# Optimization experiments

Hardware: AMD Instinct MI355X
Metric: run time of the kernel (lower is better)

## Reference

```python
import jax, jax.numpy as jnp
import numpy as np

B, H, W, D = 16, 56, 56, 384
NH, WS, SH = 12, 7, 3
HD = D // NH
N = WS * WS
nW = (H // WS) * (W // WS)
L = H * W

def _rel_pos_index():
    c = np.stack(np.meshgrid(np.arange(WS), np.arange(WS), indexing='ij')).reshape(2, -1)
    r = (c[:, :, None] - c[:, None, :]).transpose(1, 2, 0)
    r[:, :, 0] += WS - 1
    r[:, :, 1] += WS - 1
    r[:, :, 0] *= 2 * WS - 1
    return r.sum(-1)  # (N, N) int indices into bias table

RPI = _rel_pos_index()

def _attn_mask():
    img = np.zeros((H, W))
    cnt = 0
    sl = (slice(0, H - WS), slice(H - WS, H - SH), slice(H - SH, None))
    for hs in sl:
        for ws in sl:
            img[hs, ws] = cnt
            cnt += 1
    mw = img.reshape(H // WS, WS, W // WS, WS).transpose(0, 2, 1, 3).reshape(-1, N)
    am = mw[:, None, :] - mw[:, :, None]
    return np.where(am != 0, -100.0, 0.0).astype(np.float32)  # (nW, N, N)

AM = jnp.asarray(_attn_mask())

def _ln(x, g, b):
    m = jnp.mean(x, -1, keepdims=True)
    v = jnp.mean((x - m) ** 2, -1, keepdims=True)
    return (x - m) * jax.lax.rsqrt(v + 1e-5) * g + b

def _fwd(x, norm1_g, norm1_b, qkv_w, qkv_b, rpb, proj_w, proj_b, norm2_g, norm2_b,
         fc1_w, fc1_b, fc2_w, fc2_b, expand_w, exnorm_g, exnorm_b):
    def blk(x, i, shifted):
        sc = x
        h = _ln(x, norm1_g[i], norm1_b[i]).reshape(B, H, W, D)
        if shifted:
            h = jnp.roll(h, (-SH, -SH), axis=(1, 2))
        # window partition: (B*nW, N, D)
        xw = h.reshape(B, H // WS, WS, W // WS, WS, D).transpose(0, 1, 3, 2, 4, 5).reshape(-1, N, D)
        qkv = (xw @ qkv_w[i] + qkv_b[i]).reshape(-1, N, 3, NH, HD).transpose(2, 0, 3, 1, 4)
        q, k, v = qkv[0] * HD ** -0.5, qkv[1], qkv[2]
        bias = rpb[i][RPI].transpose(2, 0, 1)  # (NH, N, N)
        attn = jnp.einsum('bhid,bhjd->bhij', q, k) + bias[None]
        if shifted:
            attn = (attn.reshape(B, nW, NH, N, N) + AM[None, :, None]).reshape(-1, NH, N, N)
        attn = jax.nn.softmax(attn, axis=-1)
        o = jnp.einsum('bhij,bhjd->bhid', attn, v).transpose(0, 2, 1, 3).reshape(-1, N, D)
        o = o @ proj_w[i] + proj_b[i]
        # window reverse: (B, H, W, D)
        o = o.reshape(B, H // WS, W // WS, WS, WS, D).transpose(0, 1, 3, 2, 4, 5).reshape(B, H, W, D)
        if shifted:
            o = jnp.roll(o, (SH, SH), axis=(1, 2))
        x = sc + o.reshape(B, L, D)
        h2 = _ln(x, norm2_g[i], norm2_b[i])
        h2 = jax.nn.gelu(h2 @ fc1_w[i] + fc1_b[i], approximate=False) @ fc2_w[i] + fc2_b[i]
        return x + h2

    x = blk(x, 0, False)  # W-MSA
    x = blk(x, 1, True)   # SW-MSA
    # PatchExpand: dim -> 2*dim, pixel-shuffle 2x2, norm(dim/2)
    xe = (x @ expand_w).reshape(B, H, W, 2, 2, D // 2)
    xe = xe.transpose(0, 1, 3, 2, 4, 5).reshape(B, 4 * L, D // 2)
    return _ln(xe, exnorm_g, exnorm_b)

def setup_inputs() -> dict:
    ks = jax.random.split(jax.random.key(0), 8)
    r = lambda k, s: jax.random.normal(k, s, jnp.float32) * 0.02
    return {
        'x': jax.random.normal(ks[0], (B, L, D), jnp.float32),
        'norm1_g': jnp.ones((2, D)), 'norm1_b': jnp.zeros((2, D)),
        'qkv_w': r(ks[1], (2, D, 3 * D)), 'qkv_b': jnp.zeros((2, 3 * D)),
        'rpb': r(ks[2], (2, (2 * WS - 1) ** 2, NH)),
        'proj_w': r(ks[3], (2, D, D)), 'proj_b': jnp.zeros((2, D)),
        'norm2_g': jnp.ones((2, D)), 'norm2_b': jnp.zeros((2, D)),
        'fc1_w': r(ks[4], (2, D, 4 * D)), 'fc1_b': jnp.zeros((2, 4 * D)),
        'fc2_w': r(ks[5], (2, 4 * D, D)), 'fc2_b': jnp.zeros((2, D)),
        'expand_w': r(ks[6], (D, 2 * D)),
        'exnorm_g': jnp.ones((D // 2,)), 'exnorm_b': jnp.zeros((D // 2,)),
    }

def reference(x, norm1_g, norm1_b, qkv_w, qkv_b, rpb, proj_w, proj_b, norm2_g, norm2_b,
              fc1_w, fc1_b, fc2_w, fc2_b, expand_w, exnorm_g, exnorm_b):
    return _fwd(x, norm1_g, norm1_b, qkv_w, qkv_b, rpb, proj_w, proj_b, norm2_g, norm2_b,
                fc1_w, fc1_b, fc2_w, fc2_b, expand_w, exnorm_g, exnorm_b)
```

## Files before the change

### kernel.cpp

```cpp
#include <hip/hip_runtime.h>
#include <cstdint>
#include <cstddef>

typedef unsigned short u16;
typedef unsigned int u32;
typedef __attribute__((ext_vector_type(8))) short bf16x8;
typedef __attribute__((ext_vector_type(4))) float f32x4;

__device__ __forceinline__ float bf2f(u32 u) {
  union { u32 i; float f; } c; c.i = u << 16; return c.f;
}
__device__ __forceinline__ u16 f2bf(float f) {
  union { float f; u32 i; } c; c.f = f;
  u32 r = c.i + 0x7fffu + ((c.i >> 16) & 1u);
  return (u16)(r >> 16);
}

__device__ __forceinline__ int srcrow_map(int m, int shifted) {
  int w = m / 49, n = m - w * 49;
  int b = w >> 6, wi = w & 63;
  int wy = wi >> 3, wx = wi & 7;
  int ty = n / 7, tx = n - ty * 7;
  int h = wy * 7 + ty, x = wx * 7 + tx;
  if (shifted) { h += 3; if (h >= 56) h -= 56; x += 3; if (x >= 56) x -= 56; }
  return b * 3136 + h * 56 + x;
}

__global__ void detect_kernel(const u32* __restrict__ x, int* __restrict__ flag) {
  int t = threadIdx.x;
  int c = 0;
  for (int i = t; i < 1024; i += 256) {
    u32 e = (x[i] >> 7) & 0xFFu;
    c += (e >= 100 && e <= 130) ? 1 : 0;
  }
#pragma unroll
  for (int m = 1; m < 64; m <<= 1) c += __shfl_xor(c, m, 64);
  __shared__ int part[4];
  if ((t & 63) == 0) part[t >> 6] = c;
  __syncthreads();
  if (t == 0) flag[0] = (part[0] + part[1] + part[2] + part[3] > 700) ? 1 : 0;
}

__global__ void convert_kernel(const void* __restrict__ in, u16* __restrict__ out,
                               int n, const int* __restrict__ flag) {
  int i = blockIdx.x * 256 + threadIdx.x;
  if (i >= n) return;
  if (flag[0]) out[i] = ((const u16*)in)[i];
  else out[i] = f2bf(((const float*)in)[i]);
}

__global__ void transpose_kernel(const void* __restrict__ in, u16* __restrict__ out,
                                 int R, int C, int total, const int* __restrict__ flag) {
  int i = blockIdx.x * 256 + threadIdx.x;
  if (i >= total) return;
  int rc = R * C;
  int bb = i / rc, rem = i - bb * rc;
  int c = rem / R, r = rem - c * R;
  size_t s = (size_t)bb * rc + (size_t)r * C + c;
  out[i] = flag[0] ? ((const u16*)in)[s] : f2bf(((const float*)in)[s]);
}

__global__ __launch_bounds__(256)
void ln384_kernel(const u16* __restrict__ in, const u16* __restrict__ g,
                  const u16* __restrict__ b, u16* __restrict__ out) {
  int row = blockIdx.x * 4 + (threadIdx.x >> 6);
  int lane = threadIdx.x & 63;
  const u32* p = (const u32*)(in + (size_t)row * 384);
  float x[6]; float sum = 0.f, sq = 0.f;
#pragma unroll
  for (int j = 0; j < 3; ++j) {
    u32 u = p[lane + 64 * j];
    float a0 = bf2f(u & 0xffff), a1 = bf2f(u >> 16);
    x[2 * j] = a0; x[2 * j + 1] = a1;
    sum += a0 + a1; sq += a0 * a0 + a1 * a1;
  }
#pragma unroll
  for (int m = 1; m < 64; m <<= 1) { sum += __shfl_xor(sum, m, 64); sq += __shfl_xor(sq, m, 64); }
  float mean = sum * (1.f / 384.f);
  float var = sq * (1.f / 384.f) - mean * mean;
  float rstd = rsqrtf(var + 1e-5f);
  u32* op = (u32*)(out + (size_t)row * 384);
  const u32* g32 = (const u32*)g; const u32* b32 = (const u32*)b;
#pragma unroll
  for (int j = 0; j < 3; ++j) {
    int c = lane + 64 * j;
    u32 gg = g32[c], bb = b32[c];
    float y0 = (x[2 * j] - mean) * rstd * bf2f(gg & 0xffff) + bf2f(bb & 0xffff);
    float y1 = (x[2 * j + 1] - mean) * rstd * bf2f(gg >> 16) + bf2f(bb >> 16);
    op[c] = (u32)f2bf(y0) | ((u32)f2bf(y1) << 16);
  }
}

__global__ __launch_bounds__(256)
void lnfinal_kernel(const u16* __restrict__ in, const u16* __restrict__ g,
                    const u16* __restrict__ b, void* __restrict__ outv,
                    const int* __restrict__ flag) {
  int row = blockIdx.x * 8 + (threadIdx.x >> 5);
  int s = threadIdx.x & 31;
  int fl = flag[0];
  int bb = row / 12544, rem = row - bb * 12544;
  int hh = rem / 112, wp = rem - hh * 112;
  int h = hh >> 1, a = hh & 1, w = wp >> 1, c2 = wp & 1;
  const u32* p = (const u32*)(in + ((size_t)(bb * 3136 + h * 56 + w)) * 768 + (a * 2 + c2) * 192);
  float x[6]; float sum = 0.f, sq = 0.f;
#pragma unroll
  for (int j = 0; j < 3; ++j) {
    u32 u = p[s + 32 * j];
    float a0 = bf2f(u & 0xffff), a1 = bf2f(u >> 16);
    x[2 * j] = a0; x[2 * j + 1] = a1;
    sum += a0 + a1; sq += a0 * a0 + a1 * a1;
  }
#pragma unroll
  for (int m = 1; m < 32; m <<= 1) { sum += __shfl_xor(sum, m, 32); sq += __shfl_xor(sq, m, 32); }
  float mean = sum * (1.f / 192.f);
  float var = sq * (1.f / 192.f) - mean * mean;
  float rstd = rsqrtf(var + 1e-5f);
  const u32* g32 = (const u32*)g; const u32* b32 = (const u32*)b;
#pragma unroll
  for (int j = 0; j < 3; ++j) {
    int c = s + 32 * j;
    u32 gg = g32[c], bv = b32[c];
    float y0 = (x[2 * j] - mean) * rstd * bf2f(gg & 0xffff) + bf2f(bv & 0xffff);
    float y1 = (x[2 * j + 1] - mean) * rstd * bf2f(gg >> 16) + bf2f(bv >> 16);
    if (fl) {
      u32* op = (u32*)((u16*)outv + (size_t)row * 192);
      op[c] = (u32)f2bf(y0) | ((u32)f2bf(y1) << 16);
    } else {
      float2* op = (float2*)((float*)outv + (size_t)row * 192);
      float2 v; v.x = y0; v.y = y1;
      op[c] = v;
    }
  }
}

template <int MODE>
__global__ __launch_bounds__(256, 2)
void gemm_kernel(const u16* __restrict__ A, const u16* __restrict__ Bt,
                 const u16* __restrict__ bias, const u16* __restrict__ resid,
                 u16* __restrict__ C, int N, int K, int shifted) {
  __shared__ __attribute__((aligned(16))) char smem[16384];
  u16* As = (u16*)smem;
  u16* Bs = (u16*)(smem + 8192);

  const int t = threadIdx.x;
  const int lane = t & 63;
  const int wave = t >> 6;
  const int mblk = blockIdx.y, nblk = blockIdx.x;

  const u16* aptr[2]; const u16* bptr[2];
  char* ldsa[2]; char* ldsb[2];
#pragma unroll
  for (int i = 0; i < 2; ++i) {
    int c = t + i * 256;
    int r = c >> 2, off8 = (c & 3) * 8;
    int gr = mblk * 128 + r;
    int src = (MODE == 0) ? srcrow_map(gr, shifted) : gr;
    aptr[i] = A + (size_t)src * K + off8;
    int gn = nblk * 128 + r;
    bptr[i] = Bt + (size_t)gn * K + off8;
    ldsa[i] = smem + c * 16;
    ldsb[i] = smem + 8192 + c * 16;
  }

  f32x4 acc[4][4];
#pragma unroll
  for (int i = 0; i < 4; ++i)
#pragma unroll
    for (int j = 0; j < 4; ++j) { f32x4 z = {0.f, 0.f, 0.f, 0.f}; acc[i][j] = z; }

  const int quad = lane >> 4, l15 = lane & 15;
  const int wm = (wave >> 1) * 64, wn = (wave & 1) * 64;

  for (int kt = 0; kt < K; kt += 32) {
#pragma unroll
    for (int i = 0; i < 2; ++i) {
      __builtin_amdgcn_global_load_lds((const void*)aptr[i], (void*)ldsa[i], 16, 0, 0);
      __builtin_amdgcn_global_load_lds((const void*)bptr[i], (void*)ldsb[i], 16, 0, 0);
      aptr[i] += 32; bptr[i] += 32;
    }
    __syncthreads();
    bf16x8 af[4], bfv[4];
#pragma unroll
    for (int mt = 0; mt < 4; ++mt)
      af[mt] = *(const bf16x8*)(As + (wm + mt * 16 + l15) * 32 + quad * 8);
#pragma unroll
    for (int nt = 0; nt < 4; ++nt)
      bfv[nt] = *(const bf16x8*)(Bs + (wn + nt * 16 + l15) * 32 + quad * 8);
#pragma unroll
    for (int mt = 0; mt < 4; ++mt)
#pragma unroll
      for (int nt = 0; nt < 4; ++nt)
        acc[mt][nt] = __builtin_amdgcn_mfma_f32_16x16x32_bf16(af[mt], bfv[nt], acc[mt][nt], 0, 0, 0);
    __syncthreads();
  }

#pragma unroll
  for (int mt = 0; mt < 4; ++mt) {
#pragma unroll
    for (int r = 0; r < 4; ++r) {
      int rr = mblk * 128 + wm + mt * 16 + quad * 4 + r;
      int w49 = 0, n49 = 0, src = 0;
      if (MODE == 0) { w49 = rr / 49; n49 = rr - w49 * 49; }
      if (MODE == 1) { src = srcrow_map(rr, shifted); }
#pragma unroll
      for (int nt = 0; nt < 4; ++nt) {
        int col = nblk * 128 + wn + nt * 16 + l15;
        float v = acc[mt][nt][r];
        if (MODE == 0) {
          v += bf2f(bias[col]);
          int part = col / 384;
          int cw = col - part * 384;
          if (part == 0) v *= 0.17677669529663689f;
          int head = cw >> 5, hd = cw & 31;
          size_t idx = ((((size_t)part * 1024 + w49) * 12 + head) * 49 + n49) * 32 + hd;
          C[idx] = f2bf(v);
        } else if (MODE == 1) {
          size_t o = (size_t)src * 384 + col;
          v += bf2f(bias[col]) + bf2f(resid[o]);
          C[o] = f2bf(v);
        } else if (MODE == 2) {
          v += bf2f(bias[col]);
          v = 0.5f * v * (1.0f + erff(v * 0.70710678118654752f));
          C[(size_t)rr * (size_t)N + col] = f2bf(v);
        } else if (MODE == 3) {
          size_t o = (size_t)rr * 384 + col;
          v += bf2f(bias[col]) + bf2f(resid[o]);
          C[o] = f2bf(v);
        } else {
          C[(size_t)rr * (size_t)N + col] = f2bf(v);
        }
      }
    }
  }
}

__global__ void biastab_kernel(const u16* __restrict__ rpb, float* __restrict__ bt, int shifted) {
  int idx = blockIdx.x * 256 + threadIdx.x;
  if (idx >= 4 * 12 * 2401) return;
  int ij = idx % 2401, ch = idx / 2401;
  int head = ch % 12, cls = ch / 12;
  int i = ij / 49, j = ij % 49;
  int iy = i / 7, ix = i - iy * 7, jy = j / 7, jx = j - jy * 7;
  int rp = (iy - jy + 6) * 13 + (ix - jx + 6);
  float v = bf2f(rpb[rp * 12 + head]);
  if (shifted) {
    int clsy = cls >> 1, clsx = cls & 1;
    int regi = (clsy ? (iy < 4 ? 1 : 2) : 0) * 3 + (clsx ? (ix < 4 ? 1 : 2) : 0);
    int regj = (clsy ? (jy < 4 ? 1 : 2) : 0) * 3 + (clsx ? (jx < 4 ? 1 : 2) : 0);
    if (regi != regj) v -= 100.f;
  }
  bt[idx] = v;
}

__global__ __launch_bounds__(256, 3)
void attn_mfma_kernel(const u16* __restrict__ qkv, const float* __restrict__ bt,
                      u16* __restrict__ o) {
  __shared__ __attribute__((aligned(16))) char pbuf[4][8192];
  const int wave = threadIdx.x >> 6;
  const int lane = threadIdx.x & 63;
  const int quad = lane >> 4, l15 = lane & 15;
  const int blk = blockIdx.x * 4 + wave;
  const int w = blk / 12, head = blk - w * 12;
  const int wi = w & 63;
  const int cls = (((wi >> 3) == 7) ? 2 : 0) + (((wi & 7) == 7) ? 1 : 0);
  const float* btw = bt + (size_t)(cls * 12 + head) * 2401;
  char* pw = &pbuf[wave][0];

  const size_t base = (size_t)blk * 1568;
  const u16* qp = qkv + base;
  const u16* kp = qkv + 19267584 + base;
  const u16* vp = qkv + 2 * 19267584 + base;

  bf16x8 qf[4], kf[4];
#pragma unroll
  for (int mi = 0; mi < 4; ++mi)
    qf[mi] = *(const bf16x8*)(qp + (size_t)(mi * 16 + l15) * 32 + quad * 8);
#pragma unroll
  for (int nj = 0; nj < 4; ++nj)
    kf[nj] = *(const bf16x8*)(kp + (size_t)(nj * 16 + l15) * 32 + quad * 8);

  bf16x8 vf[2][2];
#pragma unroll
  for (int kk = 0; kk < 2; ++kk)
#pragma unroll
    for (int n2 = 0; n2 < 2; ++n2) {
      bf16x8 tv;
#pragma unroll
      for (int j = 0; j < 8; ++j) {
        int key = kk * 32 + quad * 8 + j;
        u16 raw = vp[(size_t)key * 32 + n2 * 16 + l15];
        tv[j] = (key < 49) ? (short)raw : (short)0;
      }
      vf[kk][n2] = tv;
    }

  f32x4 s[4][4];
#pragma unroll
  for (int mi = 0; mi < 4; ++mi)
#pragma unroll
    for (int nj = 0; nj < 4; ++nj) { f32x4 z = {0.f, 0.f, 0.f, 0.f}; s[mi][nj] = z; }
#pragma unroll
  for (int mi = 0; mi < 4; ++mi)
#pragma unroll
    for (int nj = 0; nj < 4; ++nj)
      s[mi][nj] = __builtin_amdgcn_mfma_f32_16x16x32_bf16(qf[mi], kf[nj], s[mi][nj], 0, 0, 0);

  const bool c3ok = (l15 == 0);
#pragma unroll
  for (int mi = 0; mi < 4; ++mi) {
#pragma unroll
    for (int r = 0; r < 4; ++r) {
      int i = mi * 16 + quad * 4 + r;
      const float* brow = btw + i * 49;
      float v0 = s[mi][0][r] + brow[l15];
      float v1 = s[mi][1][r] + brow[l15 + 16];
      float v2 = s[mi][2][r] + brow[l15 + 32];
      float v3 = c3ok ? (s[mi][3][r] + brow[48]) : -1e30f;
      float mx = fmaxf(fmaxf(v0, v1), fmaxf(v2, v3));
#pragma unroll
      for (int t = 1; t < 16; t <<= 1) mx = fmaxf(mx, __shfl_xor(mx, t, 64));
      float e0 = __expf(v0 - mx), e1 = __expf(v1 - mx);
      float e2 = __expf(v2 - mx), e3 = __expf(v3 - mx);
      float ls = e0 + e1 + e2 + e3;
#pragma unroll
      for (int t = 1; t < 16; t <<= 1) ls += __shfl_xor(ls, t, 64);
      float inv = 1.f / ls;
      u32 sw = (u32)((i & 7) << 4);
      *(u16*)(pw + (((u32)(i * 128 + l15 * 2)) ^ sw)) = f2bf(e0 * inv);
      *(u16*)(pw + (((u32)(i * 128 + (l15 + 16) * 2)) ^ sw)) = f2bf(e1 * inv);
      *(u16*)(pw + (((u32)(i * 128 + (l15 + 32) * 2)) ^ sw)) = f2bf(e2 * inv);
      *(u16*)(pw + (((u32)(i * 128 + (l15 + 48) * 2)) ^ sw)) = f2bf(e3 * inv);
    }
  }

  asm volatile("s_waitcnt lgkmcnt(0)" ::: "memory");
  __builtin_amdgcn_sched_barrier(0);

  f32x4 oacc[4][2];
#pragma unroll
  for (int mi = 0; mi < 4; ++mi)
#pragma unroll
    for (int n2 = 0; n2 < 2; ++n2) { f32x4 z = {0.f, 0.f, 0.f, 0.f}; oacc[mi][n2] = z; }
#pragma unroll
  for (int mi = 0; mi < 4; ++mi) {
#pragma unroll
    for (int kk = 0; kk < 2; ++kk) {
      int arow = mi * 16 + l15;
      u32 ab = ((u32)(arow * 128 + (kk * 32 + quad * 8) * 2)) ^ ((u32)((arow & 7) << 4));
      bf16x8 pf = *(const bf16x8*)(pw + ab);
#pragma unroll
      for (int n2 = 0; n2 < 2; ++n2)
        oacc[mi][n2] = __builtin_amdgcn_mfma_f32_16x16x32_bf16(pf, vf[kk][n2], oacc[mi][n2], 0, 0, 0);
    }
  }

#pragma unroll
  for (int mi = 0; mi < 4; ++mi)
#pragma unroll
    for (int r = 0; r < 4; ++r) {
      int row = mi * 16 + quad * 4 + r;
      if (row < 49) {
        u16* orow = o + ((size_t)(w * 49 + row)) * 384 + head * 32;
        orow[l15] = f2bf(oacc[mi][0][r]);
        orow[16 + l15] = f2bf(oacc[mi][1][r]);
      }
    }
}

extern "C" void kernel_launch(void* const* d_in, const int* in_sizes, int n_in,
                              void* d_out, int out_size, void* d_ws, size_t ws_size,
                              hipStream_t stream) {
  char* ws = (char*)d_ws;
  u16* wsA  = (u16*)ws;
  u16* wsS  = (u16*)(ws + 154140672);
  u16* wsB  = (u16*)(ws + 192675840);
  u16* wsT  = (u16*)(ws + 231211008);
  u16* wsP  = (u16*)(ws + 238878720);
  int* flag = (int*)(ws + 238907568);
  float* bt = (float*)(ws + 115736576);

  u16* qkvT  = wsT;
  u16* projT = qkvT + 2 * 442368;
  u16* fc1T  = projT + 2 * 147456;
  u16* fc2T  = fc1T + 2 * 589824;
  u16* expT  = fc2T + 2 * 589824;

  u16* p_n1g  = wsP + 0;
  u16* p_n1b  = wsP + 768;
  u16* p_qkvb = wsP + 1536;
  u16* p_rpb  = wsP + 3840;
  u16* p_prjb = wsP + 7896;
  u16* p_n2g  = wsP + 8664;
  u16* p_n2b  = wsP + 9432;
  u16* p_fc1b = wsP + 10200;
  u16* p_fc2b = wsP + 13272;
  u16* p_exg  = wsP + 14040;
  u16* p_exb  = wsP + 14232;

  detect_kernel<<<1, 256, 0, stream>>>((const u32*)d_in[0], flag);

  convert_kernel<<<(19267584 + 255) / 256, 256, 0, stream>>>(d_in[0], wsS, 19267584, flag);
  auto cv = [&](const void* src, u16* dst, int n) {
    convert_kernel<<<(n + 255) / 256, 256, 0, stream>>>(src, dst, n, flag);
  };
  cv(d_in[1],  p_n1g, 768);   cv(d_in[2],  p_n1b, 768);
  cv(d_in[4],  p_qkvb, 2304); cv(d_in[5],  p_rpb, 4056);
  cv(d_in[7],  p_prjb, 768);  cv(d_in[8],  p_n2g, 768);
  cv(d_in[9],  p_n2b, 768);   cv(d_in[11], p_fc1b, 3072);
  cv(d_in[13], p_fc2b, 768);  cv(d_in[15], p_exg, 192);
  cv(d_in[16], p_exb, 192);

  {
    int tot;
    tot = 2 * 384 * 1152; transpose_kernel<<<(tot + 255) / 256, 256, 0, stream>>>(d_in[3],  qkvT, 384, 1152, tot, flag);
    tot = 2 * 384 * 384;  transpose_kernel<<<(tot + 255) / 256, 256, 0, stream>>>(d_in[6],  projT, 384, 384,  tot, flag);
    tot = 2 * 384 * 1536; transpose_kernel<<<(tot + 255) / 256, 256, 0, stream>>>(d_in[10], fc1T, 384, 1536, tot, flag);
    tot = 2 * 1536 * 384; transpose_kernel<<<(tot + 255) / 256, 256, 0, stream>>>(d_in[12], fc2T, 1536, 384, tot, flag);
    tot = 384 * 768;      transpose_kernel<<<(tot + 255) / 256, 256, 0, stream>>>(d_in[14], expT, 384, 768,  tot, flag);
  }

  for (int i = 0; i < 2; ++i) {
    int shifted = i;
    biastab_kernel<<<451, 256, 0, stream>>>(p_rpb + i * 2028, bt, shifted);
    ln384_kernel<<<12544, 256, 0, stream>>>(wsS, p_n1g + i * 384, p_n1b + i * 384, wsB);
    gemm_kernel<0><<<dim3(9, 392), 256, 0, stream>>>(wsB, qkvT + i * 442368, p_qkvb + i * 1152,
                                                     nullptr, wsA, 1152, 384, shifted);
    attn_mfma_kernel<<<3072, 256, 0, stream>>>(wsA, bt, wsB);
    gemm_kernel<1><<<dim3(3, 392), 256, 0, stream>>>(wsB, projT + i * 147456, p_prjb + i * 384,
                                                     wsS, wsS, 384, 384, shifted);
    ln384_kernel<<<12544, 256, 0, stream>>>(wsS, p_n2g + i * 384, p_n2b + i * 384, wsB);
    gemm_kernel<2><<<dim3(12, 392), 256, 0, stream>>>(wsB, fc1T + i * 589824, p_fc1b + i * 1536,
                                                      nullptr, wsA, 1536, 384, 0);
    gemm_kernel<3><<<dim3(3, 392), 256, 0, stream>>>(wsA, fc2T + i * 589824, p_fc2b + i * 384,
                                                     wsS, wsS, 384, 1536, 0);
  }

  gemm_kernel<4><<<dim3(6, 392), 256, 0, stream>>>(wsS, expT, nullptr, nullptr, wsA, 768, 384, 0);
  lnfinal_kernel<<<25088, 256, 0, stream>>>(wsA, p_exg, p_exb, d_out, flag);
}
```

Measured before the change: 1.203 ms.

## Double-buffer GEMM LDS tiles, remap workgroups across XCDs, vectorize convert

```diff
diff --git a/kernel.cpp b/kernel.cpp
--- a/kernel.cpp
+++ b/kernel.cpp
@@ -42,11 +42,18 @@
 }
 
 __global__ void convert_kernel(const void* __restrict__ in, u16* __restrict__ out,
-                               int n, const int* __restrict__ flag) {
+                               int n4, const int* __restrict__ flag) {
   int i = blockIdx.x * 256 + threadIdx.x;
-  if (i >= n) return;
-  if (flag[0]) out[i] = ((const u16*)in)[i];
-  else out[i] = f2bf(((const float*)in)[i]);
+  if (i >= n4) return;
+  if (flag[0]) {
+    ((uint2*)out)[i] = ((const uint2*)in)[i];
+  } else {
+    float4 v = ((const float4*)in)[i];
+    uint2 r;
+    r.x = (u32)f2bf(v.x) | ((u32)f2bf(v.y) << 16);
+    r.y = (u32)f2bf(v.z) | ((u32)f2bf(v.w) << 16);
+    ((uint2*)out)[i] = r;
+  }
 }
 
 __global__ void transpose_kernel(const void* __restrict__ in, u16* __restrict__ out,
@@ -137,15 +144,15 @@
 __global__ __launch_bounds__(256, 2)
 void gemm_kernel(const u16* __restrict__ A, const u16* __restrict__ Bt,
                  const u16* __restrict__ bias, const u16* __restrict__ resid,
-                 u16* __restrict__ C, int N, int K, int shifted) {
-  __shared__ __attribute__((aligned(16))) char smem[16384];
-  u16* As = (u16*)smem;
-  u16* Bs = (u16*)(smem + 8192);
+                 u16* __restrict__ C, int N, int K, int shifted, int nn) {
+  __shared__ __attribute__((aligned(16))) char smem[32768];
 
   const int t = threadIdx.x;
   const int lane = t & 63;
   const int wave = t >> 6;
-  const int mblk = blockIdx.y, nblk = blockIdx.x;
+
+  const int wgid = (blockIdx.x & 7) * ((int)gridDim.x >> 3) + (blockIdx.x >> 3);
+  const int mblk = wgid / nn, nblk = wgid - mblk * nn;
 
   const u16* aptr[2]; const u16* bptr[2];
   char* ldsa[2]; char* ldsb[2];
@@ -171,14 +178,17 @@
   const int quad = lane >> 4, l15 = lane & 15;
   const int wm = (wave >> 1) * 64, wn = (wave & 1) * 64;
 
-  for (int kt = 0; kt < K; kt += 32) {
+  auto stage = [&](int b) {
 #pragma unroll
     for (int i = 0; i < 2; ++i) {
-      __builtin_amdgcn_global_load_lds((const void*)aptr[i], (void*)ldsa[i], 16, 0, 0);
-      __builtin_amdgcn_global_load_lds((const void*)bptr[i], (void*)ldsb[i], 16, 0, 0);
+      __builtin_amdgcn_global_load_lds((const void*)aptr[i], (void*)(ldsa[i] + b * 16384), 16, 0, 0);
+      __builtin_amdgcn_global_load_lds((const void*)bptr[i], (void*)(ldsb[i] + b * 16384), 16, 0, 0);
       aptr[i] += 32; bptr[i] += 32;
     }
-    __syncthreads();
+  };
+  auto compute = [&](int b) {
+    const u16* As = (const u16*)(smem + b * 16384);
+    const u16* Bs = (const u16*)(smem + b * 16384 + 8192);
     bf16x8 af[4], bfv[4];
 #pragma unroll
     for (int mt = 0; mt < 4; ++mt)
@@ -191,8 +201,19 @@
 #pragma unroll
       for (int nt = 0; nt < 4; ++nt)
         acc[mt][nt] = __builtin_amdgcn_mfma_f32_16x16x32_bf16(af[mt], bfv[nt], acc[mt][nt], 0, 0, 0);
+  };
+
+  const int ktiles = K >> 5;
+  stage(0);
+  __syncthreads();
+  int cur = 0;
+  for (int kt = 0; kt < ktiles - 1; ++kt) {
+    stage(cur ^ 1);
+    compute(cur);
     __syncthreads();
-  }
+    cur ^= 1;
+  }
+  compute(cur);
 
 #pragma unroll
   for (int mt = 0; mt < 4; ++mt) {
@@ -399,9 +420,9 @@
 
   detect_kernel<<<1, 256, 0, stream>>>((const u32*)d_in[0], flag);
 
-  convert_kernel<<<(19267584 + 255) / 256, 256, 0, stream>>>(d_in[0], wsS, 19267584, flag);
+  convert_kernel<<<(19267584 / 4 + 255) / 256, 256, 0, stream>>>(d_in[0], wsS, 19267584 / 4, flag);
   auto cv = [&](const void* src, u16* dst, int n) {
-    convert_kernel<<<(n + 255) / 256, 256, 0, stream>>>(src, dst, n, flag);
+    convert_kernel<<<(n / 4 + 255) / 256, 256, 0, stream>>>(src, dst, n / 4, flag);
   };
   cv(d_in[1],  p_n1g, 768);   cv(d_in[2],  p_n1b, 768);
   cv(d_in[4],  p_qkvb, 2304); cv(d_in[5],  p_rpb, 4056);
@@ -423,18 +444,18 @@
     int shifted = i;
     biastab_kernel<<<451, 256, 0, stream>>>(p_rpb + i * 2028, bt, shifted);
     ln384_kernel<<<12544, 256, 0, stream>>>(wsS, p_n1g + i * 384, p_n1b + i * 384, wsB);
-    gemm_kernel<0><<<dim3(9, 392), 256, 0, stream>>>(wsB, qkvT + i * 442368, p_qkvb + i * 1152,
-                                                     nullptr, wsA, 1152, 384, shifted);
+    gemm_kernel<0><<<3528, 256, 0, stream>>>(wsB, qkvT + i * 442368, p_qkvb + i * 1152,
+                                             nullptr, wsA, 1152, 384, shifted, 9);
     attn_mfma_kernel<<<3072, 256, 0, stream>>>(wsA, bt, wsB);
-    gemm_kernel<1><<<dim3(3, 392), 256, 0, stream>>>(wsB, projT + i * 147456, p_prjb + i * 384,
-                                                     wsS, wsS, 384, 384, shifted);
+    gemm_kernel<1><<<1176, 256, 0, stream>>>(wsB, projT + i * 147456, p_prjb + i * 384,
+                                             wsS, wsS, 384, 384, shifted, 3);
     ln384_kernel<<<12544, 256, 0, stream>>>(wsS, p_n2g + i * 384, p_n2b + i * 384, wsB);
-    gemm_kernel<2><<<dim3(12, 392), 256, 0, stream>>>(wsB, fc1T + i * 589824, p_fc1b + i * 1536,
-                                                      nullptr, wsA, 1536, 384, 0);
-    gemm_kernel<3><<<dim3(3, 392), 256, 0, stream>>>(wsA, fc2T + i * 589824, p_fc2b + i * 384,
-                                                     wsS, wsS, 384, 1536, 0);
-  }
-
-  gemm_kernel<4><<<dim3(6, 392), 256, 0, stream>>>(wsS, expT, nullptr, nullptr, wsA, 768, 384, 0);
+    gemm_kernel<2><<<4704, 256, 0, stream>>>(wsB, fc1T + i * 589824, p_fc1b + i * 1536,
+                                             nullptr, wsA, 1536, 384, 0, 12);
+    gemm_kernel<3><<<1176, 256, 0, stream>>>(wsA, fc2T + i * 589824, p_fc2b + i * 384,
+                                             wsS, wsS, 384, 1536, 0, 3);
+  }
+
+  gemm_kernel<4><<<2352, 256, 0, stream>>>(wsS, expT, nullptr, nullptr, wsA, 768, 384, 0, 6);
   lnfinal_kernel<<<25088, 256, 0, stream>>>(wsA, p_exg, p_exb, d_out, flag);
 }
```

Result: faster. 1.109 ms (-7.8%).
